# Kernel optimization log

Hardware: AMD Instinct MI355X
Metric: run time of the kernel (lower is better)

## Reference

```python
import jax, jax.numpy as jnp
import numpy as np

B, H, M, C = 64, 8, 1024, 128
MID = 64  # mid_dims[1]


def setup_inputs() -> dict:
    key = jax.random.key(0)
    ks = jax.random.split(key, 11)
    inp = {
        "query": jax.random.normal(ks[0], (B, H, C), jnp.float32),
        "key_feat": jax.random.normal(ks[1], (B, H, M, C), jnp.float32),
        "att_mask": jax.random.randint(ks[2], (B, M), 0, 2, jnp.int32),
        "value1": jax.random.normal(ks[3], (B, H, C), jnp.float32),
        "value2": jax.random.normal(ks[4], (B, H, M, C), jnp.float32),
        # MH_Linear params (kaiming-uniform-ish scale)
        "w_basic": jax.random.uniform(ks[5], (H, C, MID), jnp.float32, -1, 1) / np.sqrt(C),
        "b_basic": jax.random.uniform(ks[6], (H, MID), jnp.float32, -1, 1) / np.sqrt(C),
        "w_last": jax.random.uniform(ks[7], (H, MID, 1), jnp.float32, -1, 1) / np.sqrt(MID),
        "b_last": jax.random.uniform(ks[8], (H, 1), jnp.float32, -1, 1) / np.sqrt(MID),
        "w_last2": jax.random.uniform(ks[9], (H, MID, C), jnp.float32, -1, 1) / np.sqrt(MID),
        "b_last2": jax.random.uniform(ks[10], (H, C), jnp.float32, -1, 1) / np.sqrt(MID),
    }
    return inp


def reference(query, key_feat, att_mask, value1, value2,
              w_basic, b_basic, w_last, b_last, w_last2, b_last2):
    # att_map: [B,H,M,C] -> basic projection [B,H,M,MID] + ReLU (dropout is eval/no-op)
    att_map = query[:, :, None, :] * key_feat
    att_map = jnp.einsum('bhmi,hio->bhmo', att_map, w_basic) + b_basic[None, :, None, :]
    att_map = jax.nn.relu(att_map)

    mask_f = att_mask.astype(att_map.dtype)            # [B,M]
    m_ext = mask_f[:, None, :, None]                    # [B,1,M,1]
    # masked mean-pool over spatial dim M -> [B,H,MID]
    att_map_pool = jnp.sum(att_map * m_ext, axis=-2) / jnp.sum(m_ext, axis=-2)

    # spatial attention logits -> [B,H,M]
    alpha_spatial = (jnp.einsum('bhmi,hio->bhmo', att_map, w_last)
                     + b_last[None, :, None, :]).squeeze(-1)
    alpha_spatial = jnp.where(att_mask[:, None, :] == 0, jnp.float32(-1e9), alpha_spatial)
    alpha_spatial = jax.nn.softmax(alpha_spatial, axis=-1)

    # attend values: [B,H,M] x [B,H,M,C] -> [B,H,C]
    v2 = jnp.einsum('bhm,bhmd->bhd', alpha_spatial, value2)

    # channel gate: [B,H,MID] -> [B,H,C]
    alpha_channel = jax.nn.sigmoid(
        jnp.einsum('bhi,hio->bho', att_map_pool, w_last2) + b_last2[None])

    return value1 * v2 * alpha_channel
```

## Files before the change

kernel.cpp:

```cpp
#include <hip/hip_runtime.h>

#define NB   64
#define NH   8
#define NM   1024
#define NC   128
#define NMID 64
#define NT   256
#define TM   32
#define NTILES (NM / TM)
#define RWS  136
#define KFS  136
#define TGRAN (TM * NC / 4)

typedef __attribute__((ext_vector_type(8))) short s16x8;
typedef __attribute__((ext_vector_type(4))) short s16x4;
typedef __attribute__((ext_vector_type(4))) float f32x4;

__device__ __forceinline__ short f2bf(float x) {
    union { float f; unsigned u; } v; v.f = x;
    unsigned r = (v.u + 0x7fffu + ((v.u >> 16) & 1u)) >> 16;
    return (short)r;
}
__device__ __forceinline__ float bf2f(short s) {
    union { unsigned u; float f; } v; v.u = ((unsigned)(unsigned short)s) << 16;
    return v.f;
}

#define STAGE_KF(ST) do {                                                   \
    _Pragma("unroll")                                                       \
    for (int r_ = 0; r_ < 4; ++r_) {                                        \
        const int g_   = r_ * NT + t;                                       \
        const int row_ = g_ >> 5;                                           \
        const int gc_  = g_ & 31;                                           \
        const float a0 = (ST)[r_].x, a1 = (ST)[r_].y,                       \
                    a2 = (ST)[r_].z, a3 = (ST)[r_].w;                       \
        s16x4 h4_, l4_; short hh_;                                          \
        hh_ = f2bf(a0); h4_[0] = hh_; l4_[0] = f2bf(a0 - bf2f(hh_));        \
        hh_ = f2bf(a1); h4_[1] = hh_; l4_[1] = f2bf(a1 - bf2f(hh_));        \
        hh_ = f2bf(a2); h4_[2] = hh_; l4_[2] = f2bf(a2 - bf2f(hh_));        \
        hh_ = f2bf(a3); h4_[3] = hh_; l4_[3] = f2bf(a3 - bf2f(hh_));        \
        *(s16x4*)&kf_hi[row_ * KFS + gc_ * 4] = h4_;                        \
        *(s16x4*)&kf_lo[row_ * KFS + gc_ * 4] = l4_;                        \
    }                                                                       \
} while (0)

__global__ __launch_bounds__(NT, 2)
void scatt_kernel(const float* __restrict__ query,
                  const float* __restrict__ key_feat,
                  const int*   __restrict__ att_mask,
                  const float* __restrict__ value1,
                  const float* __restrict__ value2,
                  const float* __restrict__ w_basic,
                  const float* __restrict__ b_basic,
                  const float* __restrict__ w_last,
                  const float* __restrict__ b_last,
                  const float* __restrict__ w_last2,
                  const float* __restrict__ b_last2,
                  float* __restrict__ out)
{
    const int bh   = blockIdx.x;
    const int b    = bh >> 3;
    const int h    = bh & 7;
    const int t    = threadIdx.x;
    const int lane = t & 63;
    const int w    = t >> 6;
    const int oh   = w & 1;
    const int rt   = w >> 1;
    const int ln15 = lane & 15;
    const int lq   = lane >> 4;
    const int mg   = t >> 5;
    const int d4   = t & 31;
    const int half = lane & 32;

    __shared__ short rwT_hi[NMID * RWS];
    __shared__ short rwT_lo[NMID * RWS];
    __shared__ short kf_hi[TM * KFS];
    __shared__ short kf_lo[TM * KFS];
    __shared__ float maskf[NM];
    __shared__ float logp[2][TM];
    __shared__ float poolp[4][32];
    __shared__ float pool_s[NMID];
    __shared__ float v2part[8][NC];
    __shared__ float red[8];
    __shared__ float csum_s;

    const float*  kf  = key_feat + (size_t)bh * NM * NC;
    const float*  v2g = value2   + (size_t)bh * NM * NC;
    const float4* kf4 = (const float4*)kf;
    const float4* v24 = (const float4*)v2g;

    float4 stA[4], stV[4];
    #pragma unroll
    for (int r = 0; r < 4; ++r) stA[r] = kf4[r * NT + t];
    #pragma unroll
    for (int r = 0; r < 4; ++r) stV[r] = v24[r * NT + t];

    float cs = 0.f;
    #pragma unroll
    for (int m = t; m < NM; m += NT) {
        const int mv = att_mask[b * NM + m];
        maskf[m] = (float)mv;
        cs += (float)mv;
    }
    #pragma unroll
    for (int sh = 32; sh > 0; sh >>= 1) cs += __shfl_xor(cs, sh, 64);
    if (lane == 0) red[w] = cs;

    {
        const float* wb = w_basic + (size_t)h * NC * NMID;
        const float* qp = query + bh * NC;
        #pragma unroll 4
        for (int r = 0; r < 32; ++r) {
            const int f = r * NT + t;
            const int o = f & 63;
            const int i = f >> 6;
            const float x = qp[i] * wb[f];
            const short hi = f2bf(x);
            rwT_hi[o * RWS + i] = hi;
            rwT_lo[o * RWS + i] = f2bf(x - bf2f(hi));
        }
    }
    __syncthreads();
    if (t == 0) csum_s = red[0] + red[1] + red[2] + red[3];

    s16x8 Bh[2][4], Bl[2][4];
    #pragma unroll
    for (int otl = 0; otl < 2; ++otl) {
        const int o = oh * 32 + otl * 16 + ln15;
        #pragma unroll
        for (int ks = 0; ks < 4; ++ks) {
            const int off = o * RWS + ks * 32 + lq * 8;
            Bh[otl][ks] = *(const s16x8*)&rwT_hi[off];
            Bl[otl][ks] = *(const s16x8*)&rwT_lo[off];
        }
    }

    const int o_0 = oh * 32 + ln15;
    const int o_1 = o_0 + 16;
    const float bb0 = b_basic[h * NMID + o_0];
    const float bb1 = b_basic[h * NMID + o_1];
    const float wl0 = w_last[h * NMID + o_0];
    const float wl1 = w_last[h * NMID + o_1];
    const float bl  = b_last[h];

    float pool0 = 0.f, pool1 = 0.f;
    f32x4 accd = {0.f, 0.f, 0.f, 0.f};
    float mx_run = -1e30f;
    float s_run  = 0.f;
    const int abase = (rt * 16 + ln15) * KFS + lq * 8;

    STAGE_KF(stA);
    #pragma unroll
    for (int r = 0; r < 4; ++r) stA[r] = kf4[TGRAN + r * NT + t];
    __syncthreads();

    #pragma unroll 1
    for (int tile = 0; tile < NTILES; ++tile) {
        f32x4 acc0 = {0.f, 0.f, 0.f, 0.f};
        f32x4 acc1 = {0.f, 0.f, 0.f, 0.f};
        #pragma unroll
        for (int ks = 0; ks < 4; ++ks) {
            const s16x8 Ah = *(const s16x8*)&kf_hi[abase + ks * 32];
            const s16x8 Al = *(const s16x8*)&kf_lo[abase + ks * 32];
            acc0 = __builtin_amdgcn_mfma_f32_16x16x32_bf16(Ah, Bh[0][ks], acc0, 0, 0, 0);
            acc1 = __builtin_amdgcn_mfma_f32_16x16x32_bf16(Ah, Bh[1][ks], acc1, 0, 0, 0);
            acc0 = __builtin_amdgcn_mfma_f32_16x16x32_bf16(Al, Bh[0][ks], acc0, 0, 0, 0);
            acc1 = __builtin_amdgcn_mfma_f32_16x16x32_bf16(Al, Bh[1][ks], acc1, 0, 0, 0);
            acc0 = __builtin_amdgcn_mfma_f32_16x16x32_bf16(Ah, Bl[0][ks], acc0, 0, 0, 0);
            acc1 = __builtin_amdgcn_mfma_f32_16x16x32_bf16(Ah, Bl[1][ks], acc1, 0, 0, 0);
        }

        const int rbase = rt * 16 + lq * 4;
        float c4[4];
        #pragma unroll
        for (int reg = 0; reg < 4; ++reg) {
            const float mvf = maskf[tile * TM + rbase + reg];
            const float y0 = fmaxf(acc0[reg] + bb0, 0.f);
            const float y1 = fmaxf(acc1[reg] + bb1, 0.f);
            pool0 = fmaf(mvf, y0, pool0);
            pool1 = fmaf(mvf, y1, pool1);
            c4[reg] = fmaf(y0, wl0, y1 * wl1);
        }
        #pragma unroll
        for (int reg = 0; reg < 4; ++reg) {
            #pragma unroll
            for (int sh = 1; sh < 16; sh <<= 1) c4[reg] += __shfl_xor(c4[reg], sh, 64);
        }
        if (ln15 == 0) {
            #pragma unroll
            for (int reg = 0; reg < 4; ++reg) logp[oh][rbase + reg] = c4[reg];
        }
        __syncthreads();

        const int lrow = lane & 31;
        float lg = logp[0][lrow] + logp[1][lrow] + bl;
        lg = (maskf[tile * TM + lrow] != 0.f) ? lg : -1e9f;
        float tmax = lg;
        #pragma unroll
        for (int sh = 1; sh <= 16; sh <<= 1) tmax = fmaxf(tmax, __shfl_xor(tmax, sh, 64));
        const float nmx = fmaxf(mx_run, tmax);
        const float fre = __expf(mx_run - nmx);
        const float e   = __expf(lg - nmx);
        float es = e;
        #pragma unroll
        for (int sh = 1; sh <= 16; sh <<= 1) es += __shfl_xor(es, sh, 64);
        s_run = s_run * fre + es;
        mx_run = nmx;

        float ek[4];
        #pragma unroll
        for (int k = 0; k < 4; ++k) ek[k] = __shfl(e, half + mg + 8 * k, 64);

        accd = accd * fre;
        #pragma unroll
        for (int k = 0; k < 4; ++k) {
            accd[0] = fmaf(ek[k], stV[k].x, accd[0]);
            accd[1] = fmaf(ek[k], stV[k].y, accd[1]);
            accd[2] = fmaf(ek[k], stV[k].z, accd[2]);
            accd[3] = fmaf(ek[k], stV[k].w, accd[3]);
        }
        if (tile + 1 < NTILES) {
            #pragma unroll
            for (int r = 0; r < 4; ++r)
                stV[r] = v24[(size_t)(tile + 1) * TGRAN + r * NT + t];
        }

        if (tile + 1 < NTILES) STAGE_KF(stA);
        __syncthreads();
        if (tile + 2 < NTILES) {
            #pragma unroll
            for (int r = 0; r < 4; ++r)
                stA[r] = kf4[(size_t)(tile + 2) * TGRAN + r * NT + t];
        }
    }

    pool0 += __shfl_xor(pool0, 16, 64); pool0 += __shfl_xor(pool0, 32, 64);
    pool1 += __shfl_xor(pool1, 16, 64); pool1 += __shfl_xor(pool1, 32, 64);
    if (lane < 16) { poolp[w][lane] = pool0; poolp[w][16 + lane] = pool1; }
    ((float4*)&v2part[mg][0])[d4] = make_float4(accd[0], accd[1], accd[2], accd[3]);
    __syncthreads();

    if (t < NMID) {
        const int ohp = t >> 5, j = t & 31;
        pool_s[t] = (poolp[ohp][j] + poolp[ohp + 2][j]) / csum_s;
    }
    __syncthreads();

    if (t < NC) {
        float v2d = 0.f;
        #pragma unroll
        for (int g = 0; g < 8; ++g) v2d += v2part[g][t];
        v2d /= s_run;
        float accg = b_last2[h * NC + t];
        const float* wl2 = w_last2 + (size_t)h * NMID * NC + t;
        #pragma unroll 8
        for (int o = 0; o < NMID; ++o)
            accg = fmaf(pool_s[o], wl2[(size_t)o * NC], accg);
        const float ach = 1.f / (1.f + __expf(-accg));
        out[bh * NC + t] = value1[bh * NC + t] * v2d * ach;
    }
}

extern "C" void kernel_launch(void* const* d_in, const int* in_sizes, int n_in,
                              void* d_out, int out_size, void* d_ws, size_t ws_size,
                              hipStream_t stream) {
    (void)in_sizes; (void)n_in; (void)out_size; (void)d_ws; (void)ws_size;
    const float* query    = (const float*)d_in[0];
    const float* key_feat = (const float*)d_in[1];
    const int*   att_mask = (const int*)d_in[2];
    const float* value1   = (const float*)d_in[3];
    const float* value2   = (const float*)d_in[4];
    const float* w_basic  = (const float*)d_in[5];
    const float* b_basic  = (const float*)d_in[6];
    const float* w_last   = (const float*)d_in[7];
    const float* b_last   = (const float*)d_in[8];
    const float* w_last2  = (const float*)d_in[9];
    const float* b_last2  = (const float*)d_in[10];
    float* outp = (float*)d_out;

    scatt_kernel<<<dim3(NB * NH), dim3(NT), 0, stream>>>(
        query, key_feat, att_mask, value1, value2,
        w_basic, b_basic, w_last, b_last, w_last2, b_last2, outp);
}
```

Before: 528.7 us.

## Double block size and tile rows, alias shared buffers via union

Raises threads per block from 256 to 512 and the spatial tile from 32 to 64 rows. Each tile's softmax and row reduction now spans a full 64-lane wavefront, and the pool and v2 partials grow to 8 and 16 slices. The prologue weight buffers and the main-loop staging buffers now share one LDS union, with an added barrier after the weights are read into registers, so more blocks can fit per CU. The aim is fewer tile iterations and barriers per head plus higher occupancy, at the cost of more register pressure under the stricter launch bound of 4 blocks.

```diff
diff --git a/kernel.cpp b/kernel.cpp
--- a/kernel.cpp
+++ b/kernel.cpp
@@ -5,8 +5,8 @@
 #define NM   1024
 #define NC   128
 #define NMID 64
-#define NT   256
-#define TM   32
+#define NT   512
+#define TM   64
 #define NTILES (NM / TM)
 #define RWS  136
 #define KFS  136
@@ -44,7 +44,7 @@
     }                                                                       \
 } while (0)
 
-__global__ __launch_bounds__(NT, 2)
+__global__ __launch_bounds__(NT, 4)
 void scatt_kernel(const float* __restrict__ query,
                   const float* __restrict__ key_feat,
                   const int*   __restrict__ att_mask,
@@ -70,19 +70,33 @@
     const int lq   = lane >> 4;
     const int mg   = t >> 5;
     const int d4   = t & 31;
-    const int half = lane & 32;
-
-    __shared__ short rwT_hi[NMID * RWS];
-    __shared__ short rwT_lo[NMID * RWS];
-    __shared__ short kf_hi[TM * KFS];
-    __shared__ short kf_lo[TM * KFS];
+
+    __shared__ union __align__(16) SMem {
+        struct {
+            short rwT_hi[NMID * RWS];
+            short rwT_lo[NMID * RWS];
+        } a;
+        struct {
+            short kf_hi[TM * KFS];
+            short kf_lo[TM * KFS];
+            float v2part[16][NC];
+            float logp[2][TM];
+            float poolp[8][32];
+            float pool_s[NMID];
+        } s1;
+    } sm;
     __shared__ float maskf[NM];
-    __shared__ float logp[2][TM];
-    __shared__ float poolp[4][32];
-    __shared__ float pool_s[NMID];
-    __shared__ float v2part[8][NC];
     __shared__ float red[8];
     __shared__ float csum_s;
+
+    short* const rwT_hi = sm.a.rwT_hi;
+    short* const rwT_lo = sm.a.rwT_lo;
+    short* const kf_hi  = sm.s1.kf_hi;
+    short* const kf_lo  = sm.s1.kf_lo;
+    auto&        v2part = sm.s1.v2part;
+    auto&        logp   = sm.s1.logp;
+    auto&        poolp  = sm.s1.poolp;
+    float* const pool_s = sm.s1.pool_s;
 
     const float*  kf  = key_feat + (size_t)bh * NM * NC;
     const float*  v2g = value2   + (size_t)bh * NM * NC;
@@ -110,7 +124,7 @@
         const float* wb = w_basic + (size_t)h * NC * NMID;
         const float* qp = query + bh * NC;
         #pragma unroll 4
-        for (int r = 0; r < 32; ++r) {
+        for (int r = 0; r < NC * NMID / NT; ++r) {
             const int f = r * NT + t;
             const int o = f & 63;
             const int i = f >> 6;
@@ -121,7 +135,8 @@
         }
     }
     __syncthreads();
-    if (t == 0) csum_s = red[0] + red[1] + red[2] + red[3];
+    if (t == 0) csum_s = red[0] + red[1] + red[2] + red[3] +
+                         red[4] + red[5] + red[6] + red[7];
 
     s16x8 Bh[2][4], Bl[2][4];
     #pragma unroll
@@ -134,6 +149,7 @@
             Bl[otl][ks] = *(const s16x8*)&rwT_lo[off];
         }
     }
+    __syncthreads();
 
     const int o_0 = oh * 32 + ln15;
     const int o_1 = o_0 + 16;
@@ -192,24 +208,24 @@
         }
         __syncthreads();
 
-        const int lrow = lane & 31;
+        const int lrow = lane;
         float lg = logp[0][lrow] + logp[1][lrow] + bl;
         lg = (maskf[tile * TM + lrow] != 0.f) ? lg : -1e9f;
         float tmax = lg;
         #pragma unroll
-        for (int sh = 1; sh <= 16; sh <<= 1) tmax = fmaxf(tmax, __shfl_xor(tmax, sh, 64));
+        for (int sh = 1; sh <= 32; sh <<= 1) tmax = fmaxf(tmax, __shfl_xor(tmax, sh, 64));
         const float nmx = fmaxf(mx_run, tmax);
         const float fre = __expf(mx_run - nmx);
         const float e   = __expf(lg - nmx);
         float es = e;
         #pragma unroll
-        for (int sh = 1; sh <= 16; sh <<= 1) es += __shfl_xor(es, sh, 64);
+        for (int sh = 1; sh <= 32; sh <<= 1) es += __shfl_xor(es, sh, 64);
         s_run = s_run * fre + es;
         mx_run = nmx;
 
         float ek[4];
         #pragma unroll
-        for (int k = 0; k < 4; ++k) ek[k] = __shfl(e, half + mg + 8 * k, 64);
+        for (int k = 0; k < 4; ++k) ek[k] = __shfl(e, mg + 16 * k, 64);
 
         accd = accd * fre;
         #pragma unroll
@@ -242,14 +258,15 @@
 
     if (t < NMID) {
         const int ohp = t >> 5, j = t & 31;
-        pool_s[t] = (poolp[ohp][j] + poolp[ohp + 2][j]) / csum_s;
+        pool_s[t] = (poolp[ohp][j] + poolp[ohp + 2][j] +
+                     poolp[ohp + 4][j] + poolp[ohp + 6][j]) / csum_s;
     }
     __syncthreads();
 
     if (t < NC) {
         float v2d = 0.f;
         #pragma unroll
-        for (int g = 0; g < 8; ++g) v2d += v2part[g][t];
+        for (int g = 0; g < 16; ++g) v2d += v2part[g][t];
         v2d /= s_run;
         float accg = b_last2[h * NC + t];
         const float* wl2 = w_last2 + (size_t)h * NMID * NC + t;
```

Result: slower. 602.7 us (+14.0%).
